# Kernel tuning notes

Measured on AMD Instinct MI355X. Metric: run time of the kernel, lower is better.

## Reference

```python
import jax, jax.numpy as jnp
import numpy as np

N_NODES = 50000
N_EDGES = 800000
N_GRAPHS = 256
IN_DIM = 128
HID = 512            # hidden_layer_size
H2 = HID // 2        # 256, conv channels
H4 = HID // 4        # 128


def _linear_init(key, fan_in, fan_out):
    kw, kb = jax.random.split(key)
    bound = 1.0 / np.sqrt(fan_in)
    W = jax.random.uniform(kw, (fan_in, fan_out), minval=-bound, maxval=bound, dtype=jnp.float32)
    b = jax.random.uniform(kb, (fan_out,), minval=-bound, maxval=bound, dtype=jnp.float32)
    return W, b


def setup_inputs() -> dict:
    key = jax.random.key(0)
    ks = jax.random.split(key, 8)
    x = jax.random.normal(ks[0], (N_NODES, IN_DIM), dtype=jnp.float32)
    edge_index = jax.random.randint(ks[1], (2, N_EDGES), 0, N_NODES, dtype=jnp.int64)
    batch = jnp.sort(jax.random.randint(ks[2], (N_NODES,), 0, N_GRAPHS, dtype=jnp.int64))
    W1, b1 = _linear_init(ks[3], IN_DIM, HID)
    Wc1, bc1 = _linear_init(ks[4], HID, H2)
    Wc2, bc2 = _linear_init(ks[5], H2, H2)
    W2, b2 = _linear_init(ks[6], H2, H4)
    W3, b3 = _linear_init(ks[7], H4, 1)
    return {"x": x, "edge_index": edge_index, "batch": batch,
            "W1": W1, "b1": b1, "Wc1": Wc1, "bc1": bc1,
            "Wc2": Wc2, "bc2": bc2, "W2": W2, "b2": b2, "W3": W3, "b3": b3}


def _gcn_conv(h, W, b, src, dst, norm):
    # PyG GCNConv: out = scatter_add(norm * (h @ W)[src] -> dst) + b
    hw = h @ W                                   # [N, C_out]
    msg = norm[:, None] * hw[src]                # [E+N, C_out] gather
    agg = jax.ops.segment_sum(msg, dst, num_segments=N_NODES)  # scatter-add
    return agg + b


def reference(x, edge_index, batch, W1, b1, Wc1, bc1, Wc2, bc2, W2, b2, W3, b3):
    # --- symmetric GCN normalization with self-loops (shared by both convs) ---
    loop = jnp.arange(N_NODES, dtype=edge_index.dtype)
    src = jnp.concatenate([edge_index[0], loop])
    dst = jnp.concatenate([edge_index[1], loop])
    deg = jax.ops.segment_sum(jnp.ones_like(dst, dtype=jnp.float32), dst, num_segments=N_NODES)
    dinv = jax.lax.rsqrt(deg)                    # deg >= 1 thanks to self-loops
    norm = dinv[src] * dinv[dst]                 # [E+N]

    h = jax.nn.relu(x @ W1 + b1)                 # lin1
    h = jax.nn.relu(_gcn_conv(h, Wc1, bc1, src, dst, norm))   # conv1
    h = jax.nn.relu(_gcn_conv(h, Wc2, bc2, src, dst, norm))   # conv2

    # global_mean_pool over graph ids
    sums = jax.ops.segment_sum(h, batch, num_segments=N_GRAPHS)
    counts = jax.ops.segment_sum(jnp.ones((N_NODES,), jnp.float32), batch, num_segments=N_GRAPHS)
    g = sums / jnp.maximum(counts, 1.0)[:, None]

    # F.dropout is identity in deterministic/eval reference
    g = jax.nn.relu(g @ W2 + b2)                 # lin2
    return g @ W3 + b3                           # lin3 -> [N_GRAPHS, 1]
```

## Files before the change

kernel.cpp:

```cpp
#include <hip/hip_runtime.h>
#include <hip/hip_bf16.h>

#define NN 50000
#define NE 800000
#define NG 256
#define DIN 128
#define DH 512
#define DC 256
#define DL 128
#define NB 49

#define XBF_OFF   0UL
#define H1BF_OFF  12800000UL
#define HWBF_OFF  64000000UL
#define H2BF_OFF  89600000UL
#define H3_OFF    115200000UL
#define W1T_OFF   166400000UL
#define WC1T_OFF  166531072UL
#define WC2T_OFF  166793216UL
#define CNT_OFF   166924288UL
#define FILL_OFF  167124288UL
#define DINV_OFF  167324288UL
#define RP_OFF    167524288UL
#define BSUM_OFF  167724544UL
#define COL_OFF   167724800UL
#define EWT_OFF   170924800UL

using bf16x8 = __attribute__((ext_vector_type(8))) short;
using f32x4  = __attribute__((ext_vector_type(4))) float;

__device__ __forceinline__ short f2bf(float f) {
  unsigned u = __builtin_bit_cast(unsigned, f);
  unsigned r = u + 0x7fffu + ((u >> 16) & 1u);
  return (short)(r >> 16);
}
__device__ __forceinline__ float bf2f(unsigned short u) {
  return __builtin_bit_cast(float, (unsigned)u << 16);
}

__global__ void count_in(const int* __restrict__ dst, int* __restrict__ cnt) {
  int e = blockIdx.x * blockDim.x + threadIdx.x;
  if (e < NE) atomicAdd(&cnt[dst[e]], 1);
}

__global__ void compute_dinv(const int* __restrict__ cnt, float* __restrict__ dinv) {
  int i = blockIdx.x * blockDim.x + threadIdx.x;
  if (i < NN) dinv[i] = 1.0f / sqrtf((float)(cnt[i] + 1));
}

__global__ __launch_bounds__(1024) void scan_p1(const int* __restrict__ cnt,
                                                int* __restrict__ rowptr,
                                                int* __restrict__ bsum) {
  __shared__ int wsum[16];
  const int idx = blockIdx.x * 1024 + threadIdx.x;
  const int lane = threadIdx.x & 63, wid = threadIdx.x >> 6;
  int v = (idx < NN) ? cnt[idx] : 0;
  int incl = v;
  #pragma unroll
  for (int s = 1; s < 64; s <<= 1) {
    int t = __shfl_up(incl, s, 64);
    if (lane >= s) incl += t;
  }
  if (lane == 63) wsum[wid] = incl;
  __syncthreads();
  if (wid == 0 && lane < 16) {
    int w = wsum[lane];
    int wincl = w;
    #pragma unroll
    for (int s = 1; s < 16; s <<= 1) {
      int t = __shfl_up(wincl, s, 64);
      if (lane >= s) wincl += t;
    }
    wsum[lane] = wincl - w;
    if (lane == 15) bsum[blockIdx.x] = wincl;
  }
  __syncthreads();
  if (idx < NN) rowptr[idx] = wsum[wid] + incl - v;
}

__global__ void scan_p2(int* __restrict__ bsum, int* __restrict__ rowptr) {
  const int lane = threadIdx.x;
  int v = (lane < NB) ? bsum[lane] : 0;
  int incl = v;
  #pragma unroll
  for (int s = 1; s < 64; s <<= 1) {
    int t = __shfl_up(incl, s, 64);
    if (lane >= s) incl += t;
  }
  if (lane < NB) bsum[lane] = incl - v;
  if (lane == 63) rowptr[NN] = incl;
}

__global__ __launch_bounds__(1024) void scan_p3(int* __restrict__ rowptr,
                                                const int* __restrict__ bsum) {
  const int idx = blockIdx.x * 1024 + threadIdx.x;
  if (idx < NN && blockIdx.x > 0) rowptr[idx] += bsum[blockIdx.x];
}

__global__ void fill_csr(const int* __restrict__ src, const int* __restrict__ dst,
                         const int* __restrict__ rowptr, int* __restrict__ fill,
                         const float* __restrict__ dinv,
                         int* __restrict__ colidx, float* __restrict__ ewt) {
  int e = blockIdx.x * blockDim.x + threadIdx.x;
  if (e < NE) {
    int d = dst[e];
    int s = src[e];
    int pos = rowptr[d] + atomicAdd(&fill[d], 1);
    colidx[pos] = s;
    ewt[pos] = dinv[d] * dinv[s];
  }
}

__global__ void cvt_bf16(const float* __restrict__ in, short* __restrict__ out, int n8) {
  int i = blockIdx.x * blockDim.x + threadIdx.x;
  if (i >= n8) return;
  const float4* p = (const float4*)in + (long)i * 2;
  float4 a = p[0], b = p[1];
  bf16x8 o;
  o[0] = f2bf(a.x); o[1] = f2bf(a.y); o[2] = f2bf(a.z); o[3] = f2bf(a.w);
  o[4] = f2bf(b.x); o[5] = f2bf(b.y); o[6] = f2bf(b.z); o[7] = f2bf(b.w);
  *(bf16x8*)(out + (long)i * 8) = o;
}

__global__ void transpose_bf16(const float* __restrict__ in, short* __restrict__ out,
                               int K, int N) {
  int idx = blockIdx.x * blockDim.x + threadIdx.x;
  if (idx >= K * N) return;
  int n = idx / K, k = idx % K;
  out[idx] = f2bf(in[k * N + n]);
}

template<int OUT_BF16, int DO_RELU, int HAS_BIAS>
__global__ __launch_bounds__(256) void gemm_mfma(
    const short* __restrict__ A,
    const short* __restrict__ Bt,
    const float* __restrict__ bias,
    void* __restrict__ Cout, int M, int K, int N)
{
  __shared__ __align__(16) short As[128][40];
  __shared__ __align__(16) short Bs[128][40];
  const int tid  = threadIdx.x;
  const int lane = tid & 63;
  const int wave = tid >> 6;
  const int wr   = wave >> 1;
  const int wc   = wave & 1;
  const int bm = blockIdx.y * 128;
  const int bn = blockIdx.x * 128;

  const int sr  = tid >> 2;
  const int sc8 = (tid & 3) * 8;

  f32x4 acc[4][4];
  #pragma unroll
  for (int m = 0; m < 4; ++m)
    #pragma unroll
    for (int n = 0; n < 4; ++n)
      acc[m][n] = f32x4{0.f, 0.f, 0.f, 0.f};

  const int fr = lane & 15;
  const int kb = (lane >> 4) * 8;

  for (int k0 = 0; k0 < K; k0 += 32) {
    #pragma unroll
    for (int h = 0; h < 2; ++h) {
      int r  = sr + h * 64;
      int gm = bm + r;
      int4 av = (gm < M) ? *(const int4*)(A + (long)gm * K + k0 + sc8)
                         : int4{0, 0, 0, 0};
      *(int4*)&As[r][sc8] = av;
      int gn = bn + r;
      *(int4*)&Bs[r][sc8] = *(const int4*)(Bt + (long)gn * K + k0 + sc8);
    }
    __syncthreads();
    bf16x8 af[4], bfr[4];
    #pragma unroll
    for (int m = 0; m < 4; ++m)
      af[m] = *(const bf16x8*)&As[wr * 64 + m * 16 + fr][kb];
    #pragma unroll
    for (int n = 0; n < 4; ++n)
      bfr[n] = *(const bf16x8*)&Bs[wc * 64 + n * 16 + fr][kb];
    #pragma unroll
    for (int m = 0; m < 4; ++m)
      #pragma unroll
      for (int n = 0; n < 4; ++n)
        acc[m][n] = __builtin_amdgcn_mfma_f32_16x16x32_bf16(af[m], bfr[n], acc[m][n], 0, 0, 0);
    __syncthreads();
  }

  const int cr4 = (lane >> 4) * 4;
  const int cc  = lane & 15;
  #pragma unroll
  for (int m = 0; m < 4; ++m) {
    #pragma unroll
    for (int r = 0; r < 4; ++r) {
      int gm = bm + wr * 64 + m * 16 + cr4 + r;
      if (gm >= M) continue;
      #pragma unroll
      for (int n = 0; n < 4; ++n) {
        int gn = bn + wc * 64 + n * 16 + cc;
        float v = acc[m][n][r];
        if (HAS_BIAS) v += bias[gn];
        if (DO_RELU) v = fmaxf(v, 0.f);
        if (OUT_BF16) ((short*)Cout)[(long)gm * N + gn] = f2bf(v);
        else          ((float*)Cout)[(long)gm * N + gn] = v;
      }
    }
  }
}

template<int OUT_BF16>
__global__ __launch_bounds__(256) void aggregate_v3(
    const unsigned short* __restrict__ hw, const int* __restrict__ colidx,
    const float* __restrict__ ewt, const int* __restrict__ rowptr,
    const float* __restrict__ dinv, const float* __restrict__ bias,
    void* __restrict__ out)
{
  const int wid  = threadIdx.x >> 6;
  const int lane = threadIdx.x & 63;
  const int i = blockIdx.x * 4 + wid;
  if (i >= NN) return;
  const int c0 = lane * 4;
  const float di = dinv[i];

  ushort4 sv = *(const ushort4*)(hw + (long)i * DC + c0);
  const float dii = di * di;
  float acc0 = dii * bf2f(sv.x);
  float acc1 = dii * bf2f(sv.y);
  float acc2 = dii * bf2f(sv.z);
  float acc3 = dii * bf2f(sv.w);

  const int s0 = rowptr[i], s1 = rowptr[i + 1];
  int e = s0;
  for (; e + 8 <= s1; e += 8) {
    int nn[8]; float wv[8]; ushort4 vv[8];
    #pragma unroll
    for (int j = 0; j < 8; ++j) { nn[j] = colidx[e + j]; wv[j] = ewt[e + j]; }
    #pragma unroll
    for (int j = 0; j < 8; ++j) vv[j] = *(const ushort4*)(hw + (long)nn[j] * DC + c0);
    #pragma unroll
    for (int j = 0; j < 8; ++j) {
      acc0 += wv[j] * bf2f(vv[j].x);
      acc1 += wv[j] * bf2f(vv[j].y);
      acc2 += wv[j] * bf2f(vv[j].z);
      acc3 += wv[j] * bf2f(vv[j].w);
    }
  }
  for (; e + 4 <= s1; e += 4) {
    int nn[4]; float wv[4]; ushort4 vv[4];
    #pragma unroll
    for (int j = 0; j < 4; ++j) { nn[j] = colidx[e + j]; wv[j] = ewt[e + j]; }
    #pragma unroll
    for (int j = 0; j < 4; ++j) vv[j] = *(const ushort4*)(hw + (long)nn[j] * DC + c0);
    #pragma unroll
    for (int j = 0; j < 4; ++j) {
      acc0 += wv[j] * bf2f(vv[j].x);
      acc1 += wv[j] * bf2f(vv[j].y);
      acc2 += wv[j] * bf2f(vv[j].z);
      acc3 += wv[j] * bf2f(vv[j].w);
    }
  }
  for (; e < s1; ++e) {
    int s = colidx[e];
    float w = ewt[e];
    ushort4 v = *(const ushort4*)(hw + (long)s * DC + c0);
    acc0 += w * bf2f(v.x);
    acc1 += w * bf2f(v.y);
    acc2 += w * bf2f(v.z);
    acc3 += w * bf2f(v.w);
  }
  const float4 bv = *(const float4*)(bias + c0);
  acc0 = fmaxf(acc0 + bv.x, 0.f);
  acc1 = fmaxf(acc1 + bv.y, 0.f);
  acc2 = fmaxf(acc2 + bv.z, 0.f);
  acc3 = fmaxf(acc3 + bv.w, 0.f);
  if (OUT_BF16) {
    ushort4 o;
    o.x = (unsigned short)f2bf(acc0); o.y = (unsigned short)f2bf(acc1);
    o.z = (unsigned short)f2bf(acc2); o.w = (unsigned short)f2bf(acc3);
    *(ushort4*)((unsigned short*)out + (long)i * DC + c0) = o;
  } else {
    float4 o = {acc0, acc1, acc2, acc3};
    *(float4*)((float*)out + (long)i * DC + c0) = o;
  }
}

__global__ __launch_bounds__(256) void pool_mlp_v2(
    const float* __restrict__ h, const int* __restrict__ batch,
    const float* __restrict__ W2, const float* __restrict__ b2,
    const float* __restrict__ W3, const float* __restrict__ b3,
    float* __restrict__ out)
{
  __shared__ float part[4][DC];
  __shared__ float gmean[DC];
  __shared__ float red[DL];
  const int g = blockIdx.x;
  const int t = threadIdx.x;
  const int wid = t >> 6;
  const int lane = t & 63;
  const int c0 = lane * 4;

  int lo = 0, hi = NN;
  while (lo < hi) { int mid = (lo + hi) >> 1; if (batch[mid] < g) lo = mid + 1; else hi = mid; }
  const int start = lo;
  hi = NN;
  while (lo < hi) { int mid = (lo + hi) >> 1; if (batch[mid] < g + 1) lo = mid + 1; else hi = mid; }
  const int end = lo;

  float4 a0 = {0.f, 0.f, 0.f, 0.f}, a1 = {0.f, 0.f, 0.f, 0.f};
  int i = start + wid;
  for (; i + 4 < end; i += 8) {
    float4 v0 = *(const float4*)(h + (long)i * DC + c0);
    float4 v1 = *(const float4*)(h + (long)(i + 4) * DC + c0);
    a0.x += v0.x; a0.y += v0.y; a0.z += v0.z; a0.w += v0.w;
    a1.x += v1.x; a1.y += v1.y; a1.z += v1.z; a1.w += v1.w;
  }
  if (i < end) {
    float4 v0 = *(const float4*)(h + (long)i * DC + c0);
    a0.x += v0.x; a0.y += v0.y; a0.z += v0.z; a0.w += v0.w;
  }
  a0.x += a1.x; a0.y += a1.y; a0.z += a1.z; a0.w += a1.w;
  *(float4*)&part[wid][c0] = a0;
  __syncthreads();
  if (wid == 0) {
    const float inv = 1.0f / fmaxf((float)(end - start), 1.f);
    float4 s0 = *(const float4*)&part[0][c0];
    float4 s1 = *(const float4*)&part[1][c0];
    float4 s2 = *(const float4*)&part[2][c0];
    float4 s3 = *(const float4*)&part[3][c0];
    float4 m;
    m.x = (s0.x + s1.x + s2.x + s3.x) * inv;
    m.y = (s0.y + s1.y + s2.y + s3.y) * inv;
    m.z = (s0.z + s1.z + s2.z + s3.z) * inv;
    m.w = (s0.w + s1.w + s2.w + s3.w) * inv;
    *(float4*)&gmean[c0] = m;
  }
  __syncthreads();
  if (t < DL) {
    float acc = b2[t];
    for (int k = 0; k < DC; ++k) acc = fmaf(gmean[k], W2[k * DL + t], acc);
    red[t] = fmaxf(acc, 0.f) * W3[t];
  }
  __syncthreads();
  for (int s2 = 64; s2 > 0; s2 >>= 1) {
    if (t < s2) red[t] += red[t + s2];
    __syncthreads();
  }
  if (t == 0) out[g] = red[0] + b3[0];
}

extern "C" void kernel_launch(void* const* d_in, const int* in_sizes, int n_in,
                              void* d_out, int out_size, void* d_ws, size_t ws_size,
                              hipStream_t stream) {
  const float* x    = (const float*)d_in[0];
  const int*   ei   = (const int*)d_in[1];
  const int*   bat  = (const int*)d_in[2];
  const float* W1   = (const float*)d_in[3];
  const float* b1   = (const float*)d_in[4];
  const float* Wc1  = (const float*)d_in[5];
  const float* bc1  = (const float*)d_in[6];
  const float* Wc2  = (const float*)d_in[7];
  const float* bc2  = (const float*)d_in[8];
  const float* W2   = (const float*)d_in[9];
  const float* b2   = (const float*)d_in[10];
  const float* W3   = (const float*)d_in[11];
  const float* b3   = (const float*)d_in[12];
  float* out = (float*)d_out;

  char* ws = (char*)d_ws;
  short* xbf    = (short*)(ws + XBF_OFF);
  short* h1bf   = (short*)(ws + H1BF_OFF);
  unsigned short* hwbf = (unsigned short*)(ws + HWBF_OFF);
  unsigned short* h2bf = (unsigned short*)(ws + H2BF_OFF);
  float* h3     = (float*)(ws + H3_OFF);
  short* W1t    = (short*)(ws + W1T_OFF);
  short* Wc1t   = (short*)(ws + WC1T_OFF);
  short* Wc2t   = (short*)(ws + WC2T_OFF);
  int*   cnt    = (int*)  (ws + CNT_OFF);
  int*   fill   = (int*)  (ws + FILL_OFF);
  float* dinv   = (float*)(ws + DINV_OFF);
  int*   rowptr = (int*)  (ws + RP_OFF);
  int*   bsum   = (int*)  (ws + BSUM_OFF);
  int*   colidx = (int*)  (ws + COL_OFF);
  float* ewt    = (float*)(ws + EWT_OFF);

  const int* srcE = ei;
  const int* dstE = ei + NE;

  hipMemsetAsync(cnt, 0, 2 * NN * sizeof(int), stream);

  count_in<<<(NE + 255) / 256, 256, 0, stream>>>(dstE, cnt);
  scan_p1<<<NB, 1024, 0, stream>>>(cnt, rowptr, bsum);
  scan_p2<<<1, 64, 0, stream>>>(bsum, rowptr);
  scan_p3<<<NB, 1024, 0, stream>>>(rowptr, bsum);
  compute_dinv<<<(NN + 255) / 256, 256, 0, stream>>>(cnt, dinv);
  fill_csr<<<(NE + 255) / 256, 256, 0, stream>>>(srcE, dstE, rowptr, fill, dinv, colidx, ewt);

  cvt_bf16<<<(NN * DIN / 8 + 255) / 256, 256, 0, stream>>>(x, xbf, NN * DIN / 8);
  transpose_bf16<<<(DIN * DH + 255) / 256, 256, 0, stream>>>(W1, W1t, DIN, DH);
  transpose_bf16<<<(DH * DC + 255) / 256, 256, 0, stream>>>(Wc1, Wc1t, DH, DC);
  transpose_bf16<<<(DC * DC + 255) / 256, 256, 0, stream>>>(Wc2, Wc2t, DC, DC);

  {
    dim3 grid(DH / 128, (NN + 127) / 128);
    gemm_mfma<1, 1, 1><<<grid, 256, 0, stream>>>(xbf, W1t, b1, h1bf, NN, DIN, DH);
  }
  {
    dim3 grid(DC / 128, (NN + 127) / 128);
    gemm_mfma<1, 0, 0><<<grid, 256, 0, stream>>>(h1bf, Wc1t, nullptr, (void*)hwbf, NN, DH, DC);
  }
  aggregate_v3<1><<<(NN + 3) / 4, 256, 0, stream>>>(hwbf, colidx, ewt, rowptr, dinv, bc1, h2bf);
  {
    dim3 grid(DC / 128, (NN + 127) / 128);
    gemm_mfma<1, 0, 0><<<grid, 256, 0, stream>>>((const short*)h2bf, Wc2t, nullptr, (void*)hwbf, NN, DC, DC);
  }
  aggregate_v3<0><<<(NN + 3) / 4, 256, 0, stream>>>(hwbf, colidx, ewt, rowptr, dinv, bc2, h3);

  pool_mlp_v2<<<NG, 256, 0, stream>>>(h3, bat, W2, b2, W3, b3, out);
}
```

Baseline: 346.1 us.

## Use direct global-to-LDS GEMM loads, packed edge list, bf16 conv2 output, split aggregation

The GEMM now stages tiles with global_load_lds 16-byte transfers into unpadded LDS and drops the M-bound check. Edge source and weight are packed into one int2 array. The dinv computation is folded into the scan kernel. Aggregation has each half-wave handle alternate edges with 8-wide bf16 loads, then combines the halves with a shuffle. Conv2 output and pooling input switch from fp32 to bf16 to cut traffic. Risks include out-of-bounds reads on the last M tile (50000 is not a multiple of 128), LDS bank conflicts from removing the padding, and lower precision.

Result: slower. 364.0 us (+5.1%).

```diff
diff --git a/kernel.cpp b/kernel.cpp
--- a/kernel.cpp
+++ b/kernel.cpp
@@ -14,19 +14,19 @@
 #define H1BF_OFF  12800000UL
 #define HWBF_OFF  64000000UL
 #define H2BF_OFF  89600000UL
-#define H3_OFF    115200000UL
-#define W1T_OFF   166400000UL
-#define WC1T_OFF  166531072UL
-#define WC2T_OFF  166793216UL
-#define CNT_OFF   166924288UL
-#define FILL_OFF  167124288UL
-#define DINV_OFF  167324288UL
-#define RP_OFF    167524288UL
-#define BSUM_OFF  167724544UL
-#define COL_OFF   167724800UL
-#define EWT_OFF   170924800UL
+#define H3BF_OFF  115200000UL
+#define W1T_OFF   140800000UL
+#define WC1T_OFF  140931072UL
+#define WC2T_OFF  141193216UL
+#define CNT_OFF   141324288UL
+#define FILL_OFF  141524288UL
+#define DINV_OFF  141724288UL
+#define RP_OFF    141924288UL
+#define BSUM_OFF  142124416UL
+#define EW_OFF    142124800UL
 
 using bf16x8 = __attribute__((ext_vector_type(8))) short;
+using u16x8  = __attribute__((ext_vector_type(8))) unsigned short;
 using f32x4  = __attribute__((ext_vector_type(4))) float;
 
 __device__ __forceinline__ short f2bf(float f) {
@@ -38,19 +38,21 @@
   return __builtin_bit_cast(float, (unsigned)u << 16);
 }
 
+__device__ __forceinline__ void gload_lds16(const void* g, void* l) {
+  typedef const __attribute__((address_space(1))) unsigned gu32;
+  typedef __attribute__((address_space(3))) unsigned lu32;
+  __builtin_amdgcn_global_load_lds((gu32*)g, (lu32*)l, 16, 0, 0);
+}
+
 __global__ void count_in(const int* __restrict__ dst, int* __restrict__ cnt) {
   int e = blockIdx.x * blockDim.x + threadIdx.x;
   if (e < NE) atomicAdd(&cnt[dst[e]], 1);
 }
 
-__global__ void compute_dinv(const int* __restrict__ cnt, float* __restrict__ dinv) {
-  int i = blockIdx.x * blockDim.x + threadIdx.x;
-  if (i < NN) dinv[i] = 1.0f / sqrtf((float)(cnt[i] + 1));
-}
-
 __global__ __launch_bounds__(1024) void scan_p1(const int* __restrict__ cnt,
                                                 int* __restrict__ rowptr,
-                                                int* __restrict__ bsum) {
+                                                int* __restrict__ bsum,
+                                                float* __restrict__ dinv) {
   __shared__ int wsum[16];
   const int idx = blockIdx.x * 1024 + threadIdx.x;
   const int lane = threadIdx.x & 63, wid = threadIdx.x >> 6;
@@ -75,7 +77,10 @@
     if (lane == 15) bsum[blockIdx.x] = wincl;
   }
   __syncthreads();
-  if (idx < NN) rowptr[idx] = wsum[wid] + incl - v;
+  if (idx < NN) {
+    rowptr[idx] = wsum[wid] + incl - v;
+    dinv[idx] = 1.0f / sqrtf((float)(v + 1));
+  }
 }
 
 __global__ void scan_p2(int* __restrict__ bsum, int* __restrict__ rowptr) {
@@ -99,15 +104,13 @@
 
 __global__ void fill_csr(const int* __restrict__ src, const int* __restrict__ dst,
                          const int* __restrict__ rowptr, int* __restrict__ fill,
-                         const float* __restrict__ dinv,
-                         int* __restrict__ colidx, float* __restrict__ ewt) {
+                         const float* __restrict__ dinv, int2* __restrict__ ew) {
   int e = blockIdx.x * blockDim.x + threadIdx.x;
   if (e < NE) {
     int d = dst[e];
     int s = src[e];
     int pos = rowptr[d] + atomicAdd(&fill[d], 1);
-    colidx[pos] = s;
-    ewt[pos] = dinv[d] * dinv[s];
+    ew[pos] = make_int2(s, __float_as_int(dinv[d] * dinv[s]));
   }
 }
 
@@ -130,15 +133,15 @@
   out[idx] = f2bf(in[k * N + n]);
 }
 
-template<int OUT_BF16, int DO_RELU, int HAS_BIAS>
-__global__ __launch_bounds__(256) void gemm_mfma(
+template<int DO_RELU, int HAS_BIAS>
+__global__ __launch_bounds__(256) void gemm_mfma2(
     const short* __restrict__ A,
     const short* __restrict__ Bt,
     const float* __restrict__ bias,
-    void* __restrict__ Cout, int M, int K, int N)
+    short* __restrict__ Cout, int M, int K, int N)
 {
-  __shared__ __align__(16) short As[128][40];
-  __shared__ __align__(16) short Bs[128][40];
+  __shared__ __align__(16) short As[128][32];
+  __shared__ __align__(16) short Bs[128][32];
   const int tid  = threadIdx.x;
   const int lane = tid & 63;
   const int wave = tid >> 6;
@@ -147,8 +150,8 @@
   const int bm = blockIdx.y * 128;
   const int bn = blockIdx.x * 128;
 
-  const int sr  = tid >> 2;
-  const int sc8 = (tid & 3) * 8;
+  const int srow = lane >> 2;
+  const int scol = (lane & 3) * 8;
 
   f32x4 acc[4][4];
   #pragma unroll
@@ -162,14 +165,10 @@
 
   for (int k0 = 0; k0 < K; k0 += 32) {
     #pragma unroll
-    for (int h = 0; h < 2; ++h) {
-      int r  = sr + h * 64;
-      int gm = bm + r;
-      int4 av = (gm < M) ? *(const int4*)(A + (long)gm * K + k0 + sc8)
-                         : int4{0, 0, 0, 0};
-      *(int4*)&As[r][sc8] = av;
-      int gn = bn + r;
-      *(int4*)&Bs[r][sc8] = *(const int4*)(Bt + (long)gn * K + k0 + sc8);
+    for (int j = 0; j < 2; ++j) {
+      const int r = wave * 32 + j * 16;
+      gload_lds16(A  + (long)(bm + r + srow) * K + k0 + scol, &As[r][0]);
+      gload_lds16(Bt + (long)(bn + r + srow) * K + k0 + scol, &Bs[r][0]);
     }
     __syncthreads();
     bf16x8 af[4], bfr[4];
@@ -201,91 +200,81 @@
         float v = acc[m][n][r];
         if (HAS_BIAS) v += bias[gn];
         if (DO_RELU) v = fmaxf(v, 0.f);
-        if (OUT_BF16) ((short*)Cout)[(long)gm * N + gn] = f2bf(v);
-        else          ((float*)Cout)[(long)gm * N + gn] = v;
+        Cout[(long)gm * N + gn] = f2bf(v);
       }
     }
   }
 }
 
-template<int OUT_BF16>
-__global__ __launch_bounds__(256) void aggregate_v3(
-    const unsigned short* __restrict__ hw, const int* __restrict__ colidx,
-    const float* __restrict__ ewt, const int* __restrict__ rowptr,
-    const float* __restrict__ dinv, const float* __restrict__ bias,
-    void* __restrict__ out)
+__global__ __launch_bounds__(256) void aggregate_v4(
+    const unsigned short* __restrict__ hw, const int2* __restrict__ ew,
+    const int* __restrict__ rowptr, const float* __restrict__ dinv,
+    const float* __restrict__ bias, unsigned short* __restrict__ out)
 {
   const int wid  = threadIdx.x >> 6;
   const int lane = threadIdx.x & 63;
   const int i = blockIdx.x * 4 + wid;
   if (i >= NN) return;
-  const int c0 = lane * 4;
-  const float di = dinv[i];
-
-  ushort4 sv = *(const ushort4*)(hw + (long)i * DC + c0);
-  const float dii = di * di;
-  float acc0 = dii * bf2f(sv.x);
-  float acc1 = dii * bf2f(sv.y);
-  float acc2 = dii * bf2f(sv.z);
-  float acc3 = dii * bf2f(sv.w);
+  const int half = lane >> 5;
+  const int c0 = (lane & 31) * 8;
+
+  float acc[8] = {0.f, 0.f, 0.f, 0.f, 0.f, 0.f, 0.f, 0.f};
+  if (half == 0) {
+    const float di = dinv[i];
+    const float w = di * di;
+    u16x8 sv = *(const u16x8*)(hw + (long)i * DC + c0);
+    #pragma unroll
+    for (int k = 0; k < 8; ++k) acc[k] = w * bf2f(sv[k]);
+  }
 
   const int s0 = rowptr[i], s1 = rowptr[i + 1];
   int e = s0;
-  for (; e + 8 <= s1; e += 8) {
-    int nn[8]; float wv[8]; ushort4 vv[8];
-    #pragma unroll
-    for (int j = 0; j < 8; ++j) { nn[j] = colidx[e + j]; wv[j] = ewt[e + j]; }
-    #pragma unroll
-    for (int j = 0; j < 8; ++j) vv[j] = *(const ushort4*)(hw + (long)nn[j] * DC + c0);
+  for (; e + 16 <= s1; e += 16) {
+    int nn[8]; float wv[8]; u16x8 vv[8];
     #pragma unroll
     for (int j = 0; j < 8; ++j) {
-      acc0 += wv[j] * bf2f(vv[j].x);
-      acc1 += wv[j] * bf2f(vv[j].y);
-      acc2 += wv[j] * bf2f(vv[j].z);
-      acc3 += wv[j] * bf2f(vv[j].w);
+      int2 p = ew[e + 2 * j + half];
+      nn[j] = p.x; wv[j] = __int_as_float(p.y);
     }
-  }
-  for (; e + 4 <= s1; e += 4) {
-    int nn[4]; float wv[4]; ushort4 vv[4];
-    #pragma unroll
-    for (int j = 0; j < 4; ++j) { nn[j] = colidx[e + j]; wv[j] = ewt[e + j]; }
-    #pragma unroll
-    for (int j = 0; j < 4; ++j) vv[j] = *(const ushort4*)(hw + (long)nn[j] * DC + c0);
-    #pragma unroll
-    for (int j = 0; j < 4; ++j) {
-      acc0 += wv[j] * bf2f(vv[j].x);
-      acc1 += wv[j] * bf2f(vv[j].y);
-      acc2 += wv[j] * bf2f(vv[j].z);
-      acc3 += wv[j] * bf2f(vv[j].w);
+    #pragma unroll
+    for (int j = 0; j < 8; ++j)
+      vv[j] = *(const u16x8*)(hw + (long)nn[j] * DC + c0);
+    #pragma unroll
+    for (int j = 0; j < 8; ++j)
+      #pragma unroll
+      for (int k = 0; k < 8; ++k) acc[k] += wv[j] * bf2f(vv[j][k]);
+  }
+  for (; e + 2 <= s1; e += 2) {
+    int2 p = ew[e + half];
+    u16x8 v = *(const u16x8*)(hw + (long)p.x * DC + c0);
+    float w = __int_as_float(p.y);
+    #pragma unroll
+    for (int k = 0; k < 8; ++k) acc[k] += w * bf2f(v[k]);
+  }
+  if (e < s1 && half == 0) {
+    int2 p = ew[e];
+    u16x8 v = *(const u16x8*)(hw + (long)p.x * DC + c0);
+    float w = __int_as_float(p.y);
+    #pragma unroll
+    for (int k = 0; k < 8; ++k) acc[k] += w * bf2f(v[k]);
+  }
+
+  #pragma unroll
+  for (int k = 0; k < 8; ++k) acc[k] += __shfl_xor(acc[k], 32, 64);
+
+  if (half == 0) {
+    u16x8 o;
+    #pragma unroll
+    for (int k = 0; k < 8; ++k) {
+      float v = fmaxf(acc[k] + bias[c0 + k], 0.f);
+      o[k] = (unsigned short)f2bf(v);
     }
-  }
-  for (; e < s1; ++e) {
-    int s = colidx[e];
-    float w = ewt[e];
-    ushort4 v = *(const ushort4*)(hw + (long)s * DC + c0);
-    acc0 += w * bf2f(v.x);
-    acc1 += w * bf2f(v.y);
-    acc2 += w * bf2f(v.z);
-    acc3 += w * bf2f(v.w);
-  }
-  const float4 bv = *(const float4*)(bias + c0);
-  acc0 = fmaxf(acc0 + bv.x, 0.f);
-  acc1 = fmaxf(acc1 + bv.y, 0.f);
-  acc2 = fmaxf(acc2 + bv.z, 0.f);
-  acc3 = fmaxf(acc3 + bv.w, 0.f);
-  if (OUT_BF16) {
-    ushort4 o;
-    o.x = (unsigned short)f2bf(acc0); o.y = (unsigned short)f2bf(acc1);
-    o.z = (unsigned short)f2bf(acc2); o.w = (unsigned short)f2bf(acc3);
-    *(ushort4*)((unsigned short*)out + (long)i * DC + c0) = o;
-  } else {
-    float4 o = {acc0, acc1, acc2, acc3};
-    *(float4*)((float*)out + (long)i * DC + c0) = o;
-  }
-}
-
-__global__ __launch_bounds__(256) void pool_mlp_v2(
-    const float* __restrict__ h, const int* __restrict__ batch,
+    *(u16x8*)(out + (long)i * DC + c0) = o;
+  }
+}
+
+__global__ __launch_bounds__(256) void pool_mlp_v3(
+    const unsigned short* __restrict__ h, const int* __restrict__ batch,
     const float* __restrict__ W2, const float* __restrict__ b2,
     const float* __restrict__ W3, const float* __restrict__ b3,
     float* __restrict__ out)
@@ -309,14 +298,14 @@
   float4 a0 = {0.f, 0.f, 0.f, 0.f}, a1 = {0.f, 0.f, 0.f, 0.f};
   int i = start + wid;
   for (; i + 4 < end; i += 8) {
-    float4 v0 = *(const float4*)(h + (long)i * DC + c0);
-    float4 v1 = *(const float4*)(h + (long)(i + 4) * DC + c0);
-    a0.x += v0.x; a0.y += v0.y; a0.z += v0.z; a0.w += v0.w;
-    a1.x += v1.x; a1.y += v1.y; a1.z += v1.z; a1.w += v1.w;
+    ushort4 v0 = *(const ushort4*)(h + (long)i * DC + c0);
+    ushort4 v1 = *(const ushort4*)(h + (long)(i + 4) * DC + c0);
+    a0.x += bf2f(v0.x); a0.y += bf2f(v0.y); a0.z += bf2f(v0.z); a0.w += bf2f(v0.w);
+    a1.x += bf2f(v1.x); a1.y += bf2f(v1.y); a1.z += bf2f(v1.z); a1.w += bf2f(v1.w);
   }
   if (i < end) {
-    float4 v0 = *(const float4*)(h + (long)i * DC + c0);
-    a0.x += v0.x; a0.y += v0.y; a0.z += v0.z; a0.w += v0.w;
+    ushort4 v0 = *(const ushort4*)(h + (long)i * DC + c0);
+    a0.x += bf2f(v0.x); a0.y += bf2f(v0.y); a0.z += bf2f(v0.z); a0.w += bf2f(v0.w);
   }
   a0.x += a1.x; a0.y += a1.y; a0.z += a1.z; a0.w += a1.w;
   *(float4*)&part[wid][c0] = a0;
@@ -371,7 +360,7 @@
   short* h1bf   = (short*)(ws + H1BF_OFF);
   unsigned short* hwbf = (unsigned short*)(ws + HWBF_OFF);
   unsigned short* h2bf = (unsigned short*)(ws + H2BF_OFF);
-  float* h3     = (float*)(ws + H3_OFF);
+  unsigned short* h3bf = (unsigned short*)(ws + H3BF_OFF);
   short* W1t    = (short*)(ws + W1T_OFF);
   short* Wc1t   = (short*)(ws + WC1T_OFF);
   short* Wc2t   = (short*)(ws + WC2T_OFF);
@@ -380,8 +369,7 @@
   float* dinv   = (float*)(ws + DINV_OFF);
   int*   rowptr = (int*)  (ws + RP_OFF);
   int*   bsum   = (int*)  (ws + BSUM_OFF);
-  int*   colidx = (int*)  (ws + COL_OFF);
-  float* ewt    = (float*)(ws + EWT_OFF);
+  int2*  ew     = (int2*) (ws + EW_OFF);
 
   const int* srcE = ei;
   const int* dstE = ei + NE;
@@ -389,11 +377,10 @@
   hipMemsetAsync(cnt, 0, 2 * NN * sizeof(int), stream);
 
   count_in<<<(NE + 255) / 256, 256, 0, stream>>>(dstE, cnt);
-  scan_p1<<<NB, 1024, 0, stream>>>(cnt, rowptr, bsum);
+  scan_p1<<<NB, 1024, 0, stream>>>(cnt, rowptr, bsum, dinv);
   scan_p2<<<1, 64, 0, stream>>>(bsum, rowptr);
   scan_p3<<<NB, 1024, 0, stream>>>(rowptr, bsum);
-  compute_dinv<<<(NN + 255) / 256, 256, 0, stream>>>(cnt, dinv);
-  fill_csr<<<(NE + 255) / 256, 256, 0, stream>>>(srcE, dstE, rowptr, fill, dinv, colidx, ewt);
+  fill_csr<<<(NE + 255) / 256, 256, 0, stream>>>(srcE, dstE, rowptr, fill, dinv, ew);
 
   cvt_bf16<<<(NN * DIN / 8 + 255) / 256, 256, 0, stream>>>(x, xbf, NN * DIN / 8);
   transpose_bf16<<<(DIN * DH + 255) / 256, 256, 0, stream>>>(W1, W1t, DIN, DH);
@@ -402,18 +389,18 @@
 
   {
     dim3 grid(DH / 128, (NN + 127) / 128);
-    gemm_mfma<1, 1, 1><<<grid, 256, 0, stream>>>(xbf, W1t, b1, h1bf, NN, DIN, DH);
+    gemm_mfma2<1, 1><<<grid, 256, 0, stream>>>(xbf, W1t, b1, h1bf, NN, DIN, DH);
   }
   {
     dim3 grid(DC / 128, (NN + 127) / 128);
-    gemm_mfma<1, 0, 0><<<grid, 256, 0, stream>>>(h1bf, Wc1t, nullptr, (void*)hwbf, NN, DH, DC);
-  }
-  aggregate_v3<1><<<(NN + 3) / 4, 256, 0, stream>>>(hwbf, colidx, ewt, rowptr, dinv, bc1, h2bf);
+    gemm_mfma2<0, 0><<<grid, 256, 0, stream>>>(h1bf, Wc1t, nullptr, (short*)hwbf, NN, DH, DC);
+  }
+  aggregate_v4<<<(NN + 3) / 4, 256, 0, stream>>>(hwbf, ew, rowptr, dinv, bc1, h2bf);
   {
     dim3 grid(DC / 128, (NN + 127) / 128);
-    gemm_mfma<1, 0, 0><<<grid, 256, 0, stream>>>((const short*)h2bf, Wc2t, nullptr, (void*)hwbf, NN, DC, DC);
-  }
-  aggregate_v3<0><<<(NN + 3) / 4, 256, 0, stream>>>(hwbf, colidx, ewt, rowptr, dinv, bc2, h3);
-
-  pool_mlp_v2<<<NG, 256, 0, stream>>>(h3, bat, W2, b2, W3, b3, out);
-}
+    gemm_mfma2<0, 0><<<grid, 256, 0, stream>>>((const short*)h2bf, Wc2t, nullptr, (short*)hwbf, NN, DC, DC);
+  }
+  aggregate_v4<<<(NN + 3) / 4, 256, 0, stream>>>(hwbf, ew, rowptr, dinv, bc2, h3bf);
+
+  pool_mlp_v3<<<NG, 256, 0, stream>>>(h3bf, bat, W2, b2, W3, b3, out);
+}
```
